# Optimization experiments

Hardware: AMD Instinct MI355X
Metric: run time of the kernel (lower is better)

The kernel has to match this reference:

```python
import jax, jax.numpy as jnp
import numpy as np

MATCH_THRESH = 0.5
NEG_POS = 3
VAR0, VAR1 = 0.1, 0.2
THETA = 0.99
NEG_INF = -1e30


def point_form(c):
    # (cx, cy, w, h) -> (x1, y1, x2, y2)
    return jnp.concatenate([c[..., :2] - c[..., 2:] / 2, c[..., :2] + c[..., 2:] / 2], -1)


def iou(a, b):
    # a: [M,4] point form, b: [A,4] point form -> [M,A]
    lt = jnp.maximum(a[:, None, :2], b[None, :, :2])
    rb = jnp.minimum(a[:, None, 2:], b[None, :, 2:])
    wh = jnp.clip(rb - lt, 0.0)
    inter = wh[..., 0] * wh[..., 1]
    area_a = ((a[:, 2] - a[:, 0]) * (a[:, 3] - a[:, 1]))[:, None]
    area_b = ((b[:, 2] - b[:, 0]) * (b[:, 3] - b[:, 1]))[None, :]
    return inter / (area_a + area_b - inter)


def encode(matched, anc):
    # matched: [A,4] point-form matched GT boxes; anc: [A,4] center form
    g_cxcy = ((matched[:, :2] + matched[:, 2:]) * 0.5 - anc[:, :2]) / (VAR0 * anc[:, 2:])
    g_wh = jnp.log((matched[:, 2:] - matched[:, :2]) / anc[:, 2:]) / VAR1
    return jnp.concatenate([g_cxcy, g_wh], -1)


def match(gt_boxes, gt_labels, anc):
    # GuaranteedEncode: SSD bipartite+threshold matching with each GT guaranteed its best anchor
    M = gt_boxes.shape[0]
    ov = iou(gt_boxes, point_form(anc))  # [M, A]
    best_gt_ov = ov.max(0)               # [A]
    best_gt_idx = ov.argmax(0)           # [A]
    best_anchor = ov.argmax(1)           # [M]
    best_gt_ov = best_gt_ov.at[best_anchor].set(2.0)
    best_gt_idx = best_gt_idx.at[best_anchor].set(jnp.arange(M))
    conf = jnp.where(best_gt_ov < MATCH_THRESH, 0, gt_labels[best_gt_idx])
    loc = encode(gt_boxes[best_gt_idx], anc)
    return conf, loc


def decode(loc, anc):
    # apply ARM deltas to anchors; keep center form for re-matching
    cxcy = anc[:, :2] + loc[:, :2] * VAR0 * anc[:, 2:]
    wh = anc[:, 2:] * jnp.exp(loc[:, 2:] * VAR1)
    return jnp.concatenate([cxcy, wh], -1)


def smooth_l1(x):
    a = jnp.abs(x)
    return jnp.where(a < 1.0, 0.5 * a * a, a - 0.5)


def ce_from_logits(logits, labels):
    return -jnp.take_along_axis(jax.nn.log_softmax(logits, -1), labels[..., None], -1)[..., 0]


def setup_inputs():
    key = jax.random.key(0)
    B, A, C, M = 32, 16320, 21, 20
    ks = jax.random.split(key, 8)
    objectness = jax.random.normal(ks[0], (B, A, 2), jnp.float32)
    refine_loc = jax.random.normal(ks[1], (B, A, 4), jnp.float32)
    pred_conf = jax.random.normal(ks[2], (B, A, C), jnp.float32)
    pred_loc = jax.random.normal(ks[3], (B, A, 4), jnp.float32)
    a_cxcy = jax.random.uniform(ks[4], (1, A, 2), jnp.float32, 0.0, 1.0)
    a_wh = jax.random.uniform(ks[5], (1, A, 2), jnp.float32, 0.05, 0.5)
    anchors = jnp.concatenate([a_cxcy, a_wh], -1)  # center form
    g_cxcy = jax.random.uniform(ks[6], (B, M, 2), jnp.float32, 0.15, 0.85)
    g_wh = jax.random.uniform(ks[7], (B, M, 2), jnp.float32, 0.05, 0.3)
    gt_boxes = jnp.concatenate([g_cxcy - g_wh / 2, g_cxcy + g_wh / 2], -1)  # point form
    gt_labels = jax.random.randint(jax.random.fold_in(key, 9), (B, M), 1, C)
    return {"objectness": objectness, "refine_loc": refine_loc, "pred_conf": pred_conf,
            "pred_loc": pred_loc, "anchors": anchors, "gt_boxes": gt_boxes, "gt_labels": gt_labels}


def reference(objectness, refine_loc, pred_conf, pred_loc, anchors, gt_boxes, gt_labels):
    B, A, C = pred_conf.shape
    anc = anchors[0]
    # --- ARM stage: match GTs to fixed anchors ---
    tconf, tloc = jax.vmap(lambda gb, gl: match(gb, gl, anc))(gt_boxes, gt_labels)  # [B,A], [B,A,4]
    pos = tconf > 0
    arm_N = jnp.sum(pos).astype(jnp.float32)
    arm_loc_loss = jnp.sum(smooth_l1(refine_loc - tloc).sum(-1) * pos)
    arm_cls_loss = jnp.sum(ce_from_logits(objectness, pos.astype(jnp.int32)))
    # --- ODM stage: re-match against ARM-refined anchors, filtered by objectness ---
    object_mask = jax.nn.softmax(objectness, -1)[..., 0] < THETA  # [B,A]
    refined = jax.vmap(lambda l: decode(l, anc))(refine_loc)       # [B,A,4] center form
    tconf2, tloc2 = jax.vmap(match)(gt_boxes, gt_labels, refined)
    tloc2 = jax.lax.stop_gradient(tloc2)  # .detach() in the original
    pos2 = (tconf2 > 0) & object_mask
    N = jnp.sum(pos2).astype(jnp.float32)
    loc_loss = jnp.sum(smooth_l1(pred_loc - tloc2).sum(-1) * pos2)
    ce = ce_from_logits(pred_conf, tconf2)  # [B,A]
    pos_num = pos2.sum(-1)                  # [B]
    neg_num = jnp.maximum(10, jnp.minimum(pos_num * NEG_POS, A - pos_num))
    neg_losses = jnp.where(object_mask & (tconf2 == 0), ce, NEG_INF)
    sorted_neg = -jnp.sort(-neg_losses, axis=-1)  # descending: hard-negative mining
    take = (jnp.arange(A)[None, :] < neg_num[:, None]) & (sorted_neg > NEG_INF / 2)
    class_loss = jnp.sum(ce * pos2) + jnp.sum(jnp.where(take, sorted_neg, 0.0))
    class_loss = class_loss / N
    loc_loss = loc_loss / N
    arm_cls_loss = 0.04 * arm_cls_loss / arm_N
    arm_loc_loss = arm_loc_loss / arm_N
    total = class_loss + loc_loss + arm_cls_loss + arm_loc_loss
    return (total, class_loss, loc_loss, arm_cls_loss, arm_loc_loss)
```

## Files before the change

### kernel.cpp

```cpp
#include <hip/hip_runtime.h>
#include <math.h>

#define MATCH_THRESH 0.5f
#define THETA 0.99f
#define NEG_INF_F (-1e30f)


__device__ __forceinline__ float iou_pf(
    float ax1, float ay1, float ax2, float ay2,
    float bx1, float by1, float bx2, float by2) {
  float lx = fmaxf(ax1, bx1), ly = fmaxf(ay1, by1);
  float rx = fminf(ax2, bx2), ry = fminf(ay2, by2);
  float w = fmaxf(rx - lx, 0.f), h = fmaxf(ry - ly, 0.f);
  float inter = w * h;
  float aa = (ax2 - ax1) * (ay2 - ay1);
  float ab = (bx2 - bx1) * (by2 - by1);
  return inter / (aa + ab - inter);
}

__device__ __forceinline__ float iou_fast(
    float ax1, float ay1, float ax2, float ay2, float aa,
    float bx1, float by1, float bx2, float by2, float ab) {
  float lx = fmaxf(ax1, bx1), ly = fmaxf(ay1, by1);
  float rx = fminf(ax2, bx2), ry = fminf(ay2, by2);
  float w = fmaxf(rx - lx, 0.f), h = fmaxf(ry - ly, 0.f);
  float inter = w * h;
  return __fdividef(inter, aa + ab - inter);
}

__device__ __forceinline__ float sl1(float x) {
  float a = fabsf(x);
  return (a < 1.f) ? 0.5f * a * a : a - 0.5f;
}

__device__ __forceinline__ float wredf(float v) {
#pragma unroll
  for (int o = 32; o > 0; o >>= 1) v += __shfl_down(v, o, 64);
  return v;
}

__device__ __forceinline__ float wredmaxf(float v) {
#pragma unroll
  for (int o = 32; o > 0; o >>= 1) v = fmaxf(v, __shfl_xor(v, o, 64));
  return v;
}

__device__ __forceinline__ int wredi(int v) {
#pragma unroll
  for (int o = 32; o > 0; o >>= 1) v += __shfl_down(v, o, 64);
  return v;
}

__device__ __forceinline__ unsigned wredmaxu(unsigned v) {
#pragma unroll
  for (int o = 32; o > 0; o >>= 1) {
    unsigned ov = __shfl_down(v, o, 64);
    v = (ov > v) ? ov : v;
  }
  return v;
}

__device__ __forceinline__ unsigned long long wredmax64(unsigned long long v) {
#pragma unroll
  for (int o = 32; o > 0; o >>= 1) {
    unsigned lo = (unsigned)v, hi = (unsigned)(v >> 32);
    unsigned olo = __shfl_down(lo, o, 64);
    unsigned ohi = __shfl_down(hi, o, 64);
    unsigned long long ov = ((unsigned long long)ohi << 32) | olo;
    v = (ov > v) ? ov : v;
  }
  return v;
}

__device__ __forceinline__ unsigned fkey(float v) {
  unsigned b = __float_as_uint(v);
  return (b & 0x80000000u) ? ~b : (b | 0x80000000u);
}
__device__ __forceinline__ float keyf(unsigned u) {
  unsigned b = (u & 0x80000000u) ? (u & 0x7fffffffu) : ~u;
  return __uint_as_float(b);
}


template <int MH>
__global__ __launch_bounds__(256) void match7_kernel(
    const float* __restrict__ gt_boxes,
    const float4* __restrict__ an4,
    const float4* __restrict__ rl4all,
    unsigned long long* __restrict__ ba1p,
    unsigned long long* __restrict__ ba2p,
    int B, int A) {
  int b = blockIdx.y;
  int half = blockIdx.z;
  const float4* rl4 = rl4all + (size_t)b * A;
  int tid = threadIdx.x;

  __shared__ float sgb[MH * 4];
  __shared__ float sarea[MH];
  if (tid < MH * 4)
    sgb[tid] = gt_boxes[((size_t)b * 2 * MH + half * MH) * 4 + tid];
  __syncthreads();
  if (tid < MH)
    sarea[tid] = (sgb[tid * 4 + 2] - sgb[tid * 4]) * (sgb[tid * 4 + 3] - sgb[tid * 4 + 1]);
  __syncthreads();

  int chunk = (A + gridDim.x - 1) / gridDim.x;
  int start = blockIdx.x * chunk;
  int end = min(start + chunk, A);

  float bvA[MH], bvR[MH];
  unsigned baA[MH], baR[MH];
#pragma unroll
  for (int m = 0; m < MH; m++) {
    bvA[m] = -1.f; baA[m] = 0u;
    bvR[m] = -1.f; baR[m] = 0u;
  }

  for (int a = start + tid; a < end; a += blockDim.x) {
    float4 an = an4[a];
    float4 rl = rl4[a];
    float ax1 = an.x - an.z * 0.5f, ay1 = an.y - an.w * 0.5f;
    float ax2 = an.x + an.z * 0.5f, ay2 = an.y + an.w * 0.5f;
    float aArea = (ax2 - ax1) * (ay2 - ay1);
    float rcx = an.x + rl.x * 0.1f * an.z;
    float rcy = an.y + rl.y * 0.1f * an.w;
    float rw = an.z * expf(rl.z * 0.2f);
    float rh = an.w * expf(rl.w * 0.2f);
    float rx1 = rcx - rw * 0.5f, ry1 = rcy - rh * 0.5f;
    float rx2 = rcx + rw * 0.5f, ry2 = rcy + rh * 0.5f;
    float rArea = (rx2 - rx1) * (ry2 - ry1);

#pragma unroll
    for (int m = 0; m < MH; m++) {
      float g0 = sgb[m * 4], g1 = sgb[m * 4 + 1], g2 = sgb[m * 4 + 2], g3 = sgb[m * 4 + 3];
      float ga = sarea[m];
      float vA = iou_fast(g0, g1, g2, g3, ga, ax1, ay1, ax2, ay2, aArea);
      if (vA > bvA[m]) { bvA[m] = vA; baA[m] = (unsigned)a; }
      float vR = iou_fast(g0, g1, g2, g3, ga, rx1, ry1, rx2, ry2, rArea);
      if (vR > bvR[m]) { bvR[m] = vR; baR[m] = (unsigned)a; }
    }
  }

  bool lane0 = (tid & 63) == 0;
#pragma unroll
  for (int m = 0; m < MH; m++) {
    {
      float vmax = wredmaxf(bvA[m]);
      unsigned cand = (bvA[m] == vmax) ? ~baA[m] : 0u;
      cand = wredmaxu(cand);
      if (lane0)
        atomicMax(&ba1p[(size_t)b * 2 * MH + half * MH + m],
                  ((unsigned long long)fkey(vmax) << 32) | cand);
    }
    {
      float vmax = wredmaxf(bvR[m]);
      unsigned cand = (bvR[m] == vmax) ? ~baR[m] : 0u;
      cand = wredmaxu(cand);
      if (lane0)
        atomicMax(&ba2p[(size_t)b * 2 * MH + half * MH + m],
                  ((unsigned long long)fkey(vmax) << 32) | cand);
    }
  }
}


__global__ __launch_bounds__(256) void gt_best_kernel(
    const float* __restrict__ gt_boxes, const float4* __restrict__ an4,
    const float4* __restrict__ rl4all, unsigned long long* __restrict__ ba1p,
    unsigned long long* __restrict__ ba2p, int B, int M, int A) {
  int bm = blockIdx.y;
  int b = bm / M;
  bool refined = (blockIdx.z == 1);
  unsigned long long* dst = refined ? ba2p : ba1p;
  const float4* rl4 = rl4all + (size_t)b * A;
  const float* g = gt_boxes + (size_t)bm * 4;
  float gx1 = g[0], gy1 = g[1], gx2 = g[2], gy2 = g[3];

  int chunk = (A + gridDim.x - 1) / gridDim.x;
  int start = blockIdx.x * chunk;
  int end = min(start + chunk, A);

  unsigned long long best = 0ull;
  for (int a = start + threadIdx.x; a < end; a += blockDim.x) {
    float4 an = an4[a];
    float cx = an.x, cy = an.y, w = an.z, h = an.w;
    if (refined) {
      float4 rl = rl4[a];
      cx += rl.x * 0.1f * w;
      cy += rl.y * 0.1f * h;
      w *= expf(rl.z * 0.2f);
      h *= expf(rl.w * 0.2f);
    }
    float v = iou_pf(gx1, gy1, gx2, gy2,
                     cx - w * 0.5f, cy - h * 0.5f, cx + w * 0.5f, cy + h * 0.5f);
    unsigned long long key =
        ((unsigned long long)fkey(v) << 32) | (unsigned)(~(unsigned)a);
    if (key > best) best = key;
  }
  best = wredmax64(best);
  __shared__ unsigned long long sm[4];
  int w = threadIdx.x >> 6;
  if ((threadIdx.x & 63) == 0) sm[w] = best;
  __syncthreads();
  if (threadIdx.x == 0) {
    unsigned long long m = sm[0];
    for (int i = 1; i < 4; i++) m = (sm[i] > m) ? sm[i] : m;
    atomicMax(&dst[bm], m);
  }
}


template <int CC>
__global__ __launch_bounds__(256) void loss_kernel(
    const float* __restrict__ gt_boxes, const int* __restrict__ gt_labels,
    const float* __restrict__ anchors, const float* __restrict__ refine_loc,
    const float* __restrict__ objectness, const float* __restrict__ pred_conf,
    const float* __restrict__ pred_loc,
    const unsigned long long* __restrict__ ba1p,
    const unsigned long long* __restrict__ ba2p,
    double* __restrict__ accB,
    int* __restrict__ armNB,
    int* __restrict__ poscnt,
    float* __restrict__ negl,
    int B, int M, int A, int C) {
  __shared__ float sgb[128];
  __shared__ float sarea[32];
  __shared__ int sb1[32], sb2[32], sgl[32];
  __shared__ float sf[4][4];
  __shared__ int sw[2][4];

  int b = blockIdx.y;
  int tid = threadIdx.x;
  if (tid < M) {
    sb1[tid] = (int)(~(unsigned)ba1p[(size_t)b * M + tid]);
    sb2[tid] = (int)(~(unsigned)ba2p[(size_t)b * M + tid]);
    sgl[tid] = gt_labels[(size_t)b * M + tid];
  }
  if (tid < M * 4) sgb[tid] = gt_boxes[(size_t)b * M * 4 + tid];
  __syncthreads();
  if (tid < M)
    sarea[tid] = (sgb[tid * 4 + 2] - sgb[tid * 4]) * (sgb[tid * 4 + 3] - sgb[tid * 4 + 1]);
  __syncthreads();

  float p_arm_loc = 0.f, p_arm_cls = 0.f, p_loc = 0.f, p_cepos = 0.f;
  int p_armN = 0, p_pos2 = 0;

  int stride = gridDim.x * blockDim.x;
#pragma unroll 2
  for (int a = blockIdx.x * blockDim.x + tid; a < A; a += stride) {
    float pr[CC > 0 ? CC : 1];
    const float* pc = pred_conf + ((size_t)b * A + a) * C;
    if constexpr (CC > 0) {
#pragma unroll
      for (int c = 0; c < CC; c++) pr[c] = pc[c];
    }
    size_t idx = (size_t)b * A + a;
    float4 an = ((const float4*)anchors)[a];
    float4 rl = ((const float4*)refine_loc)[idx];
    float2 ob = ((const float2*)objectness)[idx];

    float rcx = an.x + rl.x * 0.1f * an.z;
    float rcy = an.y + rl.y * 0.1f * an.w;
    float rw = an.z * expf(rl.z * 0.2f);
    float rh = an.w * expf(rl.w * 0.2f);

    float ax1 = an.x - an.z * 0.5f, ay1 = an.y - an.w * 0.5f;
    float ax2 = an.x + an.z * 0.5f, ay2 = an.y + an.w * 0.5f;
    float aArea = (ax2 - ax1) * (ay2 - ay1);
    float rx1 = rcx - rw * 0.5f, ry1 = rcy - rh * 0.5f;
    float rx2 = rcx + rw * 0.5f, ry2 = rcy + rh * 0.5f;
    float rArea = (rx2 - rx1) * (ry2 - ry1);
    float bestA = -1.f, bestR = -1.f;
    int biA = 0, biR = 0;
    for (int m = 0; m < M; m++) {
      float g0 = sgb[m * 4], g1 = sgb[m * 4 + 1], g2 = sgb[m * 4 + 2], g3 = sgb[m * 4 + 3];
      float ga = sarea[m];
      float vA = iou_fast(g0, g1, g2, g3, ga, ax1, ay1, ax2, ay2, aArea);
      if (vA > bestA) { bestA = vA; biA = m; }
      float vR = iou_fast(g0, g1, g2, g3, ga, rx1, ry1, rx2, ry2, rArea);
      if (vR > bestR) { bestR = vR; biR = m; }
    }
    for (int m = 0; m < M; m++) {
      if (sb1[m] == a) { biA = m; bestA = 2.f; }
      if (sb2[m] == a) { biR = m; bestR = 2.f; }
    }
    int conf1 = (bestA < MATCH_THRESH) ? 0 : sgl[biA];
    int conf2 = (bestR < MATCH_THRESH) ? 0 : sgl[biR];
    int pos1 = conf1 > 0;

    if (pos1) {
      const float* g = sgb + biA * 4;
      float gcx = ((g[0] + g[2]) * 0.5f - an.x) / (0.1f * an.z);
      float gcy = ((g[1] + g[3]) * 0.5f - an.y) / (0.1f * an.w);
      float gw = logf((g[2] - g[0]) / an.z) / 0.2f;
      float gh = logf((g[3] - g[1]) / an.w) / 0.2f;
      p_arm_loc += sl1(rl.x - gcx) + sl1(rl.y - gcy) + sl1(rl.z - gw) + sl1(rl.w - gh);
    }
    float mx = fmaxf(ob.x, ob.y);
    float e0 = __expf(ob.x - mx), e1 = __expf(ob.y - mx);
    float lse = mx + __logf(e0 + e1);
    p_arm_cls += lse - (pos1 ? ob.y : ob.x);
    p_armN += pos1;

    bool mask = (e0 / (e0 + e1)) < THETA;
    int pos2 = (conf2 > 0) && mask;

    float ce;
    if constexpr (CC > 0) {
      float mxc = pr[0];
#pragma unroll
      for (int c = 1; c < CC; c++) mxc = fmaxf(mxc, pr[c]);
      float s = 0.f;
#pragma unroll
      for (int c = 0; c < CC; c++) s += __expf(pr[c] - mxc);
      float sel = pr[0];
#pragma unroll
      for (int c = 1; c < CC; c++) sel = (conf2 == c) ? pr[c] : sel;
      ce = mxc + __logf(s) - sel;
    } else {
      float mxc = pc[0];
      float s = 1.f;
      for (int c = 1; c < C; c++) {
        float v = pc[c];
        float nm = fmaxf(mxc, v);
        s = s * __expf(mxc - nm) + __expf(v - nm);
        mxc = nm;
      }
      ce = mxc + __logf(s) - pc[conf2];
    }

    if (pos2) {
      const float* g = sgb + biR * 4;
      float gcx = ((g[0] + g[2]) * 0.5f - rcx) / (0.1f * rw);
      float gcy = ((g[1] + g[3]) * 0.5f - rcy) / (0.1f * rh);
      float gw = logf((g[2] - g[0]) / rw) / 0.2f;
      float gh = logf((g[3] - g[1]) / rh) / 0.2f;
      float4 pl = ((const float4*)pred_loc)[idx];
      p_loc += sl1(pl.x - gcx) + sl1(pl.y - gcy) + sl1(pl.z - gw) + sl1(pl.w - gh);
      p_cepos += ce;
      p_pos2 += 1;
    }
    negl[idx] = (mask && conf2 == 0) ? fmaxf(ce, 0.f) : NEG_INF_F;
  }

  p_arm_loc = wredf(p_arm_loc); p_arm_cls = wredf(p_arm_cls);
  p_loc = wredf(p_loc); p_cepos = wredf(p_cepos);
  p_armN = wredi(p_armN); p_pos2 = wredi(p_pos2);
  int w = tid >> 6;
  if ((tid & 63) == 0) {
    sf[0][w] = p_arm_loc; sf[1][w] = p_arm_cls; sf[2][w] = p_loc; sf[3][w] = p_cepos;
    sw[0][w] = p_armN; sw[1][w] = p_pos2;
  }
  __syncthreads();
  if (tid == 0) {
    float aL = 0, aC = 0, oL = 0, oC = 0;
    int aN = 0, p2 = 0;
    for (int i = 0; i < 4; i++) {
      aL += sf[0][i]; aC += sf[1][i]; oL += sf[2][i]; oC += sf[3][i];
      aN += sw[0][i]; p2 += sw[1][i];
    }
    double* ab = accB + (size_t)b * 8;
    if (aL != 0.f) atomicAdd(&ab[0], (double)aL);
    atomicAdd(&ab[1], (double)aC);
    if (oL != 0.f) atomicAdd(&ab[2], (double)oL);
    if (oC != 0.f) atomicAdd(&ab[3], (double)oC);
    if (aN) atomicAdd(&armNB[b], aN);
    if (p2) atomicAdd(&poscnt[b], p2);
  }
}


__global__ __launch_bounds__(1024) void hardneg_kernel(
    const float* __restrict__ negl, const int* __restrict__ poscnt,
    const double* __restrict__ accB, const int* __restrict__ armNB,
    double* __restrict__ acc4, int* __restrict__ ctr,
    int B, int A, float* __restrict__ out) {
  int b = blockIdx.x;
  const float* nl = negl + (size_t)b * A;
  int t = threadIdx.x;
  unsigned key[16];
#pragma unroll
  for (int j = 0; j < 16; j++) {
    int i = j * 1024 + t;
    key[j] = (i < A) ? fkey(nl[i]) : 0u;
  }
  __shared__ int wcnt[2][16];
  __shared__ float wsum[16];
  __shared__ unsigned wmax[16];
  int w = t >> 6;
  bool lane0 = (t & 63) == 0;

  const unsigned UVALID = fkey(-5e29f);
  int cv = 0;
  unsigned mk = 0;
#pragma unroll
  for (int j = 0; j < 16; j++) {
    cv += (key[j] > UVALID) ? 1 : 0;
    mk = (key[j] > mk) ? key[j] : mk;
  }
  cv = wredi(cv);
  mk = wredmaxu(mk);
  if (lane0) { wcnt[0][w] = cv; wmax[w] = mk; }
  __syncthreads();
  int cnt_valid = 0;
  unsigned maxkey = 0;
  for (int i = 0; i < 16; i++) {
    cnt_valid += wcnt[0][i];
    maxkey = (wmax[i] > maxkey) ? wmax[i] : maxkey;
  }

  int pn = poscnt[b];
  int nn = max(10, min(pn * 3, A - pn));
  int K = min(nn, cnt_valid);

  if (K > 0) {
    unsigned lo = 0x7fffffffu;
    unsigned hi = (maxkey > lo) ? maxkey : lo;
    int par = 1;
    while (lo < hi) {
      unsigned d = hi - lo;
      unsigned mid = lo + (d >> 1) + (d & 1u);
      int c = 0;
#pragma unroll
      for (int j = 0; j < 16; j++) c += (key[j] >= mid) ? 1 : 0;
      c = wredi(c);
      if (lane0) wcnt[par][w] = c;
      __syncthreads();
      int tot = 0;
      for (int i = 0; i < 16; i++) tot += wcnt[par][i];
      par ^= 1;
      if (tot >= K) {
        lo = mid;
        if (tot == K) break;
      } else hi = mid - 1;
    }

    float kth = keyf(lo);
    float sum = 0.f;
    int c1 = 0;
#pragma unroll
    for (int j = 0; j < 16; j++)
      if (key[j] > lo) { sum += keyf(key[j]); c1++; }
    sum = wredf(sum);
    c1 = wredi(c1);
    __syncthreads();
    if (lane0) { wsum[w] = sum; wcnt[0][w] = c1; }
    __syncthreads();
    if (t == 0) {
      float S = 0.f;
      int C1 = 0;
      for (int i = 0; i < 16; i++) { S += wsum[i]; C1 += wcnt[0][i]; }
      S += (float)(K - C1) * kth;
      atomicAdd(acc4, (double)S);
    }
  }

  if (t == 0) {
    __threadfence();
    int old = atomicAdd(ctr, 1);
    if (old == B - 1) {
      __threadfence();
      double arm_loc = 0, arm_cls = 0, odm_loc = 0, ce_pos = 0;
      long long Ni = 0, aNi = 0;
      for (int bb = 0; bb < B; bb++) {
        const double* ab = accB + (size_t)bb * 8;
        arm_loc += ab[0]; arm_cls += ab[1]; odm_loc += ab[2]; ce_pos += ab[3];
        Ni += poscnt[bb]; aNi += armNB[bb];
      }
      double neg_sum = *acc4;
      double N = (double)Ni, armN = (double)aNi;
      double class_loss = (ce_pos + neg_sum) / N;
      double loc_loss = odm_loc / N;
      double acls = 0.04 * arm_cls / armN;
      double aloc = arm_loc / armN;
      out[0] = (float)(class_loss + loc_loss + acls + aloc);
      out[1] = (float)class_loss;
      out[2] = (float)loc_loss;
      out[3] = (float)acls;
      out[4] = (float)aloc;
    }
  }
}


extern "C" void kernel_launch(void* const* d_in, const int* in_sizes, int n_in,
                              void* d_out, int out_size, void* d_ws, size_t ws_size,
                              hipStream_t stream) {
  const float* objectness = (const float*)d_in[0];
  const float* refine_loc = (const float*)d_in[1];
  const float* pred_conf  = (const float*)d_in[2];
  const float* pred_loc   = (const float*)d_in[3];
  const float* anchors    = (const float*)d_in[4];
  const float* gt_boxes   = (const float*)d_in[5];
  const int*   gt_labels  = (const int*)d_in[6];

  int A = in_sizes[4] / 4;
  int B = in_sizes[0] / (A * 2);
  int C = (int)(in_sizes[2] / ((long long)B * A));
  int M = in_sizes[5] / (B * 4);

  char* ws = (char*)d_ws;
  double* acc4 = (double*)ws;
  int* poscnt = (int*)(ws + 64);
  int* armNB = (int*)(ws + 192);
  int* ctr = (int*)(ws + 320);
  double* accB = (double*)(ws + 512);
  size_t ba_off = 512 + (size_t)B * 64;
  unsigned long long* ba1p = (unsigned long long*)(ws + ba_off);
  unsigned long long* ba2p = (unsigned long long*)(ws + ba_off + (size_t)B * M * 8);
  size_t zero_end = ba_off + 2 * (size_t)B * M * 8;
  size_t negl_off = (zero_end + 255) & ~(size_t)255;
  float* negl = (float*)(ws + negl_off);

  bool fast = (C == 21) && (M == 20) && (B <= 32);

  hipMemsetAsync(d_ws, 0, zero_end, stream);

  if (fast) {
    dim3 mg(16, B, 2);
    match7_kernel<10><<<mg, 256, 0, stream>>>(gt_boxes, (const float4*)anchors,
                                              (const float4*)refine_loc,
                                              ba1p, ba2p, B, A);
  } else {
    dim3 gbg(4, B * M, 2);
    gt_best_kernel<<<gbg, 256, 0, stream>>>(gt_boxes, (const float4*)anchors,
                                            (const float4*)refine_loc, ba1p, ba2p, B, M, A);
  }

  dim3 grid(32, B);
  if (C == 21) {
    loss_kernel<21><<<grid, 256, 0, stream>>>(
        gt_boxes, gt_labels, anchors, refine_loc, objectness, pred_conf, pred_loc,
        ba1p, ba2p, accB, armNB, poscnt, negl, B, M, A, C);
  } else {
    loss_kernel<0><<<grid, 256, 0, stream>>>(
        gt_boxes, gt_labels, anchors, refine_loc, objectness, pred_conf, pred_loc,
        ba1p, ba2p, accB, armNB, poscnt, negl, B, M, A, C);
  }

  hardneg_kernel<<<B, 1024, 0, stream>>>(negl, poscnt, accB, armNB, acc4, ctr,
                                         B, A, (float*)d_out);
}
```

Baseline: 111.8 us.

## Fuse matching into loss pass and correct forced best-anchor matches in fixup kernel

Folds the per-GT best-anchor search into the main loss kernel, so anchors and refine_loc are read and IoUs computed once instead of in two passes. The loss is first computed from plain threshold matching. A small fixup kernel then adjusts the accumulators and negl for each GT's forced best anchor, applying deltas for loc, class, counts and negative masking. This removes one full kernel and its memory traffic. In exchange the fused kernel holds 80 per-GT tracking registers plus 21 logits, which raises register pressure and may lower occupancy, and the delta-correction logic is more fragile.

```diff
diff --git a/kernel.cpp b/kernel.cpp
--- a/kernel.cpp
+++ b/kernel.cpp
@@ -82,46 +82,253 @@
 }
 
 
-template <int MH>
-__global__ __launch_bounds__(256) void match7_kernel(
-    const float* __restrict__ gt_boxes,
-    const float4* __restrict__ an4,
-    const float4* __restrict__ rl4all,
+template <int CC, int MM>
+__global__ __launch_bounds__(256) void lossmatch_kernel(
+    const float* __restrict__ gt_boxes, const int* __restrict__ gt_labels,
+    const float* __restrict__ anchors, const float* __restrict__ refine_loc,
+    const float* __restrict__ objectness, const float* __restrict__ pred_conf,
+    const float* __restrict__ pred_loc,
     unsigned long long* __restrict__ ba1p,
     unsigned long long* __restrict__ ba2p,
+    double* __restrict__ accB,
+    int* __restrict__ armNB,
+    int* __restrict__ poscnt,
+    float* __restrict__ negl,
     int B, int A) {
+  __shared__ float sgb[MM * 4];
+  __shared__ float sarea[MM];
+  __shared__ int sgl[MM];
+  __shared__ float sf[4][4];
+  __shared__ int sw[2][4];
+
   int b = blockIdx.y;
-  int half = blockIdx.z;
-  const float4* rl4 = rl4all + (size_t)b * A;
   int tid = threadIdx.x;
-
-  __shared__ float sgb[MH * 4];
-  __shared__ float sarea[MH];
-  if (tid < MH * 4)
-    sgb[tid] = gt_boxes[((size_t)b * 2 * MH + half * MH) * 4 + tid];
-  __syncthreads();
-  if (tid < MH)
+  if (tid < MM) sgl[tid] = gt_labels[(size_t)b * MM + tid];
+  if (tid < MM * 4) sgb[tid] = gt_boxes[(size_t)b * MM * 4 + tid];
+  __syncthreads();
+  if (tid < MM)
     sarea[tid] = (sgb[tid * 4 + 2] - sgb[tid * 4]) * (sgb[tid * 4 + 3] - sgb[tid * 4 + 1]);
   __syncthreads();
 
-  int chunk = (A + gridDim.x - 1) / gridDim.x;
-  int start = blockIdx.x * chunk;
-  int end = min(start + chunk, A);
-
-  float bvA[MH], bvR[MH];
-  unsigned baA[MH], baR[MH];
-#pragma unroll
-  for (int m = 0; m < MH; m++) {
+  float p_arm_loc = 0.f, p_arm_cls = 0.f, p_loc = 0.f, p_cepos = 0.f;
+  int p_armN = 0, p_pos2 = 0;
+
+  float bvA[MM], bvR[MM];
+  unsigned baA[MM], baR[MM];
+#pragma unroll
+  for (int m = 0; m < MM; m++) {
     bvA[m] = -1.f; baA[m] = 0u;
     bvR[m] = -1.f; baR[m] = 0u;
   }
 
-  for (int a = start + tid; a < end; a += blockDim.x) {
-    float4 an = an4[a];
-    float4 rl = rl4[a];
+  int stride = gridDim.x * blockDim.x;
+  for (int a = blockIdx.x * blockDim.x + tid; a < A; a += stride) {
+    float pr[CC];
+    const float* pc = pred_conf + ((size_t)b * A + a) * CC;
+#pragma unroll
+    for (int c = 0; c < CC; c++) pr[c] = pc[c];
+
+    size_t idx = (size_t)b * A + a;
+    float4 an = ((const float4*)anchors)[a];
+    float4 rl = ((const float4*)refine_loc)[idx];
+    float2 ob = ((const float2*)objectness)[idx];
+
+    float rcx = an.x + rl.x * 0.1f * an.z;
+    float rcy = an.y + rl.y * 0.1f * an.w;
+    float rw = an.z * expf(rl.z * 0.2f);
+    float rh = an.w * expf(rl.w * 0.2f);
+
     float ax1 = an.x - an.z * 0.5f, ay1 = an.y - an.w * 0.5f;
     float ax2 = an.x + an.z * 0.5f, ay2 = an.y + an.w * 0.5f;
     float aArea = (ax2 - ax1) * (ay2 - ay1);
+    float rx1 = rcx - rw * 0.5f, ry1 = rcy - rh * 0.5f;
+    float rx2 = rcx + rw * 0.5f, ry2 = rcy + rh * 0.5f;
+    float rArea = (rx2 - rx1) * (ry2 - ry1);
+
+    float bestA = -1.f, bestR = -1.f;
+    int biA = 0, biR = 0;
+#pragma unroll
+    for (int m = 0; m < MM; m++) {
+      float g0 = sgb[m * 4], g1 = sgb[m * 4 + 1], g2 = sgb[m * 4 + 2], g3 = sgb[m * 4 + 3];
+      float ga = sarea[m];
+      float vA = iou_fast(g0, g1, g2, g3, ga, ax1, ay1, ax2, ay2, aArea);
+      if (vA > bestA) { bestA = vA; biA = m; }
+      if (vA > bvA[m]) { bvA[m] = vA; baA[m] = (unsigned)a; }
+      float vR = iou_fast(g0, g1, g2, g3, ga, rx1, ry1, rx2, ry2, rArea);
+      if (vR > bestR) { bestR = vR; biR = m; }
+      if (vR > bvR[m]) { bvR[m] = vR; baR[m] = (unsigned)a; }
+    }
+    int conf1 = (bestA < MATCH_THRESH) ? 0 : sgl[biA];
+    int conf2 = (bestR < MATCH_THRESH) ? 0 : sgl[biR];
+    int pos1 = conf1 > 0;
+
+    if (pos1) {
+      const float* g = sgb + biA * 4;
+      float gcx = ((g[0] + g[2]) * 0.5f - an.x) / (0.1f * an.z);
+      float gcy = ((g[1] + g[3]) * 0.5f - an.y) / (0.1f * an.w);
+      float gw = logf((g[2] - g[0]) / an.z) / 0.2f;
+      float gh = logf((g[3] - g[1]) / an.w) / 0.2f;
+      p_arm_loc += sl1(rl.x - gcx) + sl1(rl.y - gcy) + sl1(rl.z - gw) + sl1(rl.w - gh);
+    }
+    float mx = fmaxf(ob.x, ob.y);
+    float e0 = __expf(ob.x - mx), e1 = __expf(ob.y - mx);
+    float lse = mx + __logf(e0 + e1);
+    p_arm_cls += lse - (pos1 ? ob.y : ob.x);
+    p_armN += pos1;
+
+    bool mask = (e0 / (e0 + e1)) < THETA;
+    int pos2 = (conf2 > 0) && mask;
+
+    float mxc = pr[0];
+#pragma unroll
+    for (int c = 1; c < CC; c++) mxc = fmaxf(mxc, pr[c]);
+    float s = 0.f;
+#pragma unroll
+    for (int c = 0; c < CC; c++) s += __expf(pr[c] - mxc);
+    float sel = pr[0];
+#pragma unroll
+    for (int c = 1; c < CC; c++) sel = (conf2 == c) ? pr[c] : sel;
+    float ce = mxc + __logf(s) - sel;
+
+    if (pos2) {
+      const float* g = sgb + biR * 4;
+      float gcx = ((g[0] + g[2]) * 0.5f - rcx) / (0.1f * rw);
+      float gcy = ((g[1] + g[3]) * 0.5f - rcy) / (0.1f * rh);
+      float gw = logf((g[2] - g[0]) / rw) / 0.2f;
+      float gh = logf((g[3] - g[1]) / rh) / 0.2f;
+      float4 pl = ((const float4*)pred_loc)[idx];
+      p_loc += sl1(pl.x - gcx) + sl1(pl.y - gcy) + sl1(pl.z - gw) + sl1(pl.w - gh);
+      p_cepos += ce;
+      p_pos2 += 1;
+    }
+    negl[idx] = (mask && conf2 == 0) ? fmaxf(ce, 0.f) : NEG_INF_F;
+  }
+
+  p_arm_loc = wredf(p_arm_loc); p_arm_cls = wredf(p_arm_cls);
+  p_loc = wredf(p_loc); p_cepos = wredf(p_cepos);
+  p_armN = wredi(p_armN); p_pos2 = wredi(p_pos2);
+  int w = tid >> 6;
+  if ((tid & 63) == 0) {
+    sf[0][w] = p_arm_loc; sf[1][w] = p_arm_cls; sf[2][w] = p_loc; sf[3][w] = p_cepos;
+    sw[0][w] = p_armN; sw[1][w] = p_pos2;
+  }
+  __syncthreads();
+  if (tid == 0) {
+    float aL = 0, aC = 0, oL = 0, oC = 0;
+    int aN = 0, p2 = 0;
+    for (int i = 0; i < 4; i++) {
+      aL += sf[0][i]; aC += sf[1][i]; oL += sf[2][i]; oC += sf[3][i];
+      aN += sw[0][i]; p2 += sw[1][i];
+    }
+    double* ab = accB + (size_t)b * 8;
+    if (aL != 0.f) atomicAdd(&ab[0], (double)aL);
+    atomicAdd(&ab[1], (double)aC);
+    if (oL != 0.f) atomicAdd(&ab[2], (double)oL);
+    if (oC != 0.f) atomicAdd(&ab[3], (double)oC);
+    if (aN) atomicAdd(&armNB[b], aN);
+    if (p2) atomicAdd(&poscnt[b], p2);
+  }
+
+  bool lane0 = (tid & 63) == 0;
+#pragma unroll
+  for (int m = 0; m < MM; m++) {
+    {
+      float vmax = wredmaxf(bvA[m]);
+      unsigned cand = (bvA[m] == vmax) ? ~baA[m] : 0u;
+      cand = wredmaxu(cand);
+      if (lane0)
+        atomicMax(&ba1p[(size_t)b * MM + m],
+                  ((unsigned long long)fkey(vmax) << 32) | cand);
+    }
+    {
+      float vmax = wredmaxf(bvR[m]);
+      unsigned cand = (bvR[m] == vmax) ? ~baR[m] : 0u;
+      cand = wredmaxu(cand);
+      if (lane0)
+        atomicMax(&ba2p[(size_t)b * MM + m],
+                  ((unsigned long long)fkey(vmax) << 32) | cand);
+    }
+  }
+}
+
+
+template <int CC, int MM>
+__global__ void fixup_kernel(
+    const float* __restrict__ gt_boxes, const int* __restrict__ gt_labels,
+    const float* __restrict__ anchors, const float* __restrict__ refine_loc,
+    const float* __restrict__ objectness, const float* __restrict__ pred_conf,
+    const float* __restrict__ pred_loc,
+    const unsigned long long* __restrict__ ba1p,
+    const unsigned long long* __restrict__ ba2p,
+    double* __restrict__ accB, int* __restrict__ armNB, int* __restrict__ poscnt,
+    float* __restrict__ negl, int B, int A) {
+  int b = blockIdx.x;
+  int stage = blockIdx.y;
+  int tid = threadIdx.x;
+  __shared__ float sgb[MM * 4];
+  __shared__ float sarea[MM];
+  __shared__ int sgl[MM];
+  __shared__ int sa[MM];
+  const unsigned long long* bap = (stage ? ba2p : ba1p) + (size_t)b * MM;
+  if (tid < MM * 4) sgb[tid] = gt_boxes[(size_t)b * MM * 4 + tid];
+  if (tid < MM) {
+    sgl[tid] = gt_labels[(size_t)b * MM + tid];
+    sa[tid] = (int)(~(unsigned)bap[tid]);
+  }
+  __syncthreads();
+  if (tid < MM)
+    sarea[tid] = (sgb[tid * 4 + 2] - sgb[tid * 4]) * (sgb[tid * 4 + 3] - sgb[tid * 4 + 1]);
+  __syncthreads();
+  if (tid >= MM) return;
+  int a = sa[tid];
+  for (int m2 = tid + 1; m2 < MM; m2++)
+    if (sa[m2] == a) return;
+
+  size_t idx = (size_t)b * A + a;
+  float4 an = ((const float4*)anchors)[a];
+  float4 rl = ((const float4*)refine_loc)[idx];
+  float2 ob = ((const float2*)objectness)[idx];
+  float mx = fmaxf(ob.x, ob.y);
+  float e0 = __expf(ob.x - mx), e1 = __expf(ob.y - mx);
+
+  if (stage == 0) {
+    float ax1 = an.x - an.z * 0.5f, ay1 = an.y - an.w * 0.5f;
+    float ax2 = an.x + an.z * 0.5f, ay2 = an.y + an.w * 0.5f;
+    float aArea = (ax2 - ax1) * (ay2 - ay1);
+    float bestA = -1.f;
+    int biA = 0;
+#pragma unroll
+    for (int m = 0; m < MM; m++) {
+      float vA = iou_fast(sgb[m * 4], sgb[m * 4 + 1], sgb[m * 4 + 2], sgb[m * 4 + 3],
+                          sarea[m], ax1, ay1, ax2, ay2, aArea);
+      if (vA > bestA) { bestA = vA; biA = m; }
+    }
+    int conf1b = (bestA < MATCH_THRESH) ? 0 : sgl[biA];
+    int p1b = conf1b > 0;
+    float locB = 0.f;
+    if (p1b) {
+      const float* g = sgb + biA * 4;
+      float gcx = ((g[0] + g[2]) * 0.5f - an.x) / (0.1f * an.z);
+      float gcy = ((g[1] + g[3]) * 0.5f - an.y) / (0.1f * an.w);
+      float gw = logf((g[2] - g[0]) / an.z) / 0.2f;
+      float gh = logf((g[3] - g[1]) / an.w) / 0.2f;
+      locB = sl1(rl.x - gcx) + sl1(rl.y - gcy) + sl1(rl.z - gw) + sl1(rl.w - gh);
+    }
+    float locA;
+    {
+      const float* g = sgb + tid * 4;
+      float gcx = ((g[0] + g[2]) * 0.5f - an.x) / (0.1f * an.z);
+      float gcy = ((g[1] + g[3]) * 0.5f - an.y) / (0.1f * an.w);
+      float gw = logf((g[2] - g[0]) / an.z) / 0.2f;
+      float gh = logf((g[3] - g[1]) / an.w) / 0.2f;
+      locA = sl1(rl.x - gcx) + sl1(rl.y - gcy) + sl1(rl.z - gw) + sl1(rl.w - gh);
+    }
+    float clsDelta = (p1b ? ob.y : ob.x) - ob.y;
+    double* ab = accB + (size_t)b * 8;
+    atomicAdd(&ab[0], (double)(locA - locB));
+    if (clsDelta != 0.f) atomicAdd(&ab[1], (double)clsDelta);
+    if (!p1b) atomicAdd(&armNB[b], 1);
+  } else {
     float rcx = an.x + rl.x * 0.1f * an.z;
     float rcy = an.y + rl.y * 0.1f * an.w;
     float rw = an.z * expf(rl.z * 0.2f);
@@ -129,37 +336,66 @@
     float rx1 = rcx - rw * 0.5f, ry1 = rcy - rh * 0.5f;
     float rx2 = rcx + rw * 0.5f, ry2 = rcy + rh * 0.5f;
     float rArea = (rx2 - rx1) * (ry2 - ry1);
-
-#pragma unroll
-    for (int m = 0; m < MH; m++) {
-      float g0 = sgb[m * 4], g1 = sgb[m * 4 + 1], g2 = sgb[m * 4 + 2], g3 = sgb[m * 4 + 3];
-      float ga = sarea[m];
-      float vA = iou_fast(g0, g1, g2, g3, ga, ax1, ay1, ax2, ay2, aArea);
-      if (vA > bvA[m]) { bvA[m] = vA; baA[m] = (unsigned)a; }
-      float vR = iou_fast(g0, g1, g2, g3, ga, rx1, ry1, rx2, ry2, rArea);
-      if (vR > bvR[m]) { bvR[m] = vR; baR[m] = (unsigned)a; }
-    }
-  }
-
-  bool lane0 = (tid & 63) == 0;
-#pragma unroll
-  for (int m = 0; m < MH; m++) {
-    {
-      float vmax = wredmaxf(bvA[m]);
-      unsigned cand = (bvA[m] == vmax) ? ~baA[m] : 0u;
-      cand = wredmaxu(cand);
-      if (lane0)
-        atomicMax(&ba1p[(size_t)b * 2 * MH + half * MH + m],
-                  ((unsigned long long)fkey(vmax) << 32) | cand);
-    }
-    {
-      float vmax = wredmaxf(bvR[m]);
-      unsigned cand = (bvR[m] == vmax) ? ~baR[m] : 0u;
-      cand = wredmaxu(cand);
-      if (lane0)
-        atomicMax(&ba2p[(size_t)b * 2 * MH + half * MH + m],
-                  ((unsigned long long)fkey(vmax) << 32) | cand);
-    }
+    float bestR = -1.f;
+    int biR = 0;
+#pragma unroll
+    for (int m = 0; m < MM; m++) {
+      float vR = iou_fast(sgb[m * 4], sgb[m * 4 + 1], sgb[m * 4 + 2], sgb[m * 4 + 3],
+                          sarea[m], rx1, ry1, rx2, ry2, rArea);
+      if (vR > bestR) { bestR = vR; biR = m; }
+    }
+    int conf2b = (bestR < MATCH_THRESH) ? 0 : sgl[biR];
+    bool mask = (e0 / (e0 + e1)) < THETA;
+    int p2b = (conf2b > 0) && mask;
+    int p2a = mask ? 1 : 0;
+
+    float pr[CC];
+    const float* pc = pred_conf + idx * CC;
+#pragma unroll
+    for (int c = 0; c < CC; c++) pr[c] = pc[c];
+    float mxc = pr[0];
+#pragma unroll
+    for (int c = 1; c < CC; c++) mxc = fmaxf(mxc, pr[c]);
+    float s = 0.f;
+#pragma unroll
+    for (int c = 0; c < CC; c++) s += __expf(pr[c] - mxc);
+    float lse21 = mxc + __logf(s);
+    float selB = pr[0], selA = pr[0];
+    int conf2a = sgl[tid];
+#pragma unroll
+    for (int c = 1; c < CC; c++) {
+      selB = (conf2b == c) ? pr[c] : selB;
+      selA = (conf2a == c) ? pr[c] : selA;
+    }
+    float ceb = lse21 - selB;
+    float cea = lse21 - selA;
+
+    float locB = 0.f, locA = 0.f;
+    float4 pl = ((const float4*)pred_loc)[idx];
+    if (p2b) {
+      const float* g = sgb + biR * 4;
+      float gcx = ((g[0] + g[2]) * 0.5f - rcx) / (0.1f * rw);
+      float gcy = ((g[1] + g[3]) * 0.5f - rcy) / (0.1f * rh);
+      float gw = logf((g[2] - g[0]) / rw) / 0.2f;
+      float gh = logf((g[3] - g[1]) / rh) / 0.2f;
+      locB = sl1(pl.x - gcx) + sl1(pl.y - gcy) + sl1(pl.z - gw) + sl1(pl.w - gh);
+    }
+    if (p2a) {
+      const float* g = sgb + tid * 4;
+      float gcx = ((g[0] + g[2]) * 0.5f - rcx) / (0.1f * rw);
+      float gcy = ((g[1] + g[3]) * 0.5f - rcy) / (0.1f * rh);
+      float gw = logf((g[2] - g[0]) / rw) / 0.2f;
+      float gh = logf((g[3] - g[1]) / rh) / 0.2f;
+      locA = sl1(pl.x - gcx) + sl1(pl.y - gcy) + sl1(pl.z - gw) + sl1(pl.w - gh);
+    }
+    float dLoc = locA - locB;
+    float dCe = (p2a ? cea : 0.f) - (p2b ? ceb : 0.f);
+    int dP = p2a - p2b;
+    double* ab = accB + (size_t)b * 8;
+    if (dLoc != 0.f) atomicAdd(&ab[2], (double)dLoc);
+    if (dCe != 0.f) atomicAdd(&ab[3], (double)dCe);
+    if (dP) atomicAdd(&poscnt[b], dP);
+    negl[idx] = NEG_INF_F;
   }
 }
 
@@ -209,22 +445,16 @@
   }
 }
 
-
-template <int CC>
-__global__ __launch_bounds__(256) void loss_kernel(
+__global__ __launch_bounds__(256) void loss_fb_kernel(
     const float* __restrict__ gt_boxes, const int* __restrict__ gt_labels,
     const float* __restrict__ anchors, const float* __restrict__ refine_loc,
     const float* __restrict__ objectness, const float* __restrict__ pred_conf,
     const float* __restrict__ pred_loc,
     const unsigned long long* __restrict__ ba1p,
     const unsigned long long* __restrict__ ba2p,
-    double* __restrict__ accB,
-    int* __restrict__ armNB,
-    int* __restrict__ poscnt,
-    float* __restrict__ negl,
-    int B, int M, int A, int C) {
+    double* __restrict__ accB, int* __restrict__ armNB, int* __restrict__ poscnt,
+    float* __restrict__ negl, int B, int M, int A, int C) {
   __shared__ float sgb[128];
-  __shared__ float sarea[32];
   __shared__ int sb1[32], sb2[32], sgl[32];
   __shared__ float sf[4][4];
   __shared__ int sw[2][4];
@@ -238,23 +468,14 @@
   }
   if (tid < M * 4) sgb[tid] = gt_boxes[(size_t)b * M * 4 + tid];
   __syncthreads();
-  if (tid < M)
-    sarea[tid] = (sgb[tid * 4 + 2] - sgb[tid * 4]) * (sgb[tid * 4 + 3] - sgb[tid * 4 + 1]);
-  __syncthreads();
 
   float p_arm_loc = 0.f, p_arm_cls = 0.f, p_loc = 0.f, p_cepos = 0.f;
   int p_armN = 0, p_pos2 = 0;
 
   int stride = gridDim.x * blockDim.x;
-#pragma unroll 2
   for (int a = blockIdx.x * blockDim.x + tid; a < A; a += stride) {
-    float pr[CC > 0 ? CC : 1];
-    const float* pc = pred_conf + ((size_t)b * A + a) * C;
-    if constexpr (CC > 0) {
-#pragma unroll
-      for (int c = 0; c < CC; c++) pr[c] = pc[c];
-    }
     size_t idx = (size_t)b * A + a;
+    const float* pc = pred_conf + idx * C;
     float4 an = ((const float4*)anchors)[a];
     float4 rl = ((const float4*)refine_loc)[idx];
     float2 ob = ((const float2*)objectness)[idx];
@@ -266,18 +487,15 @@
 
     float ax1 = an.x - an.z * 0.5f, ay1 = an.y - an.w * 0.5f;
     float ax2 = an.x + an.z * 0.5f, ay2 = an.y + an.w * 0.5f;
-    float aArea = (ax2 - ax1) * (ay2 - ay1);
     float rx1 = rcx - rw * 0.5f, ry1 = rcy - rh * 0.5f;
     float rx2 = rcx + rw * 0.5f, ry2 = rcy + rh * 0.5f;
-    float rArea = (rx2 - rx1) * (ry2 - ry1);
     float bestA = -1.f, bestR = -1.f;
     int biA = 0, biR = 0;
     for (int m = 0; m < M; m++) {
       float g0 = sgb[m * 4], g1 = sgb[m * 4 + 1], g2 = sgb[m * 4 + 2], g3 = sgb[m * 4 + 3];
-      float ga = sarea[m];
-      float vA = iou_fast(g0, g1, g2, g3, ga, ax1, ay1, ax2, ay2, aArea);
+      float vA = iou_pf(g0, g1, g2, g3, ax1, ay1, ax2, ay2);
       if (vA > bestA) { bestA = vA; biA = m; }
-      float vR = iou_fast(g0, g1, g2, g3, ga, rx1, ry1, rx2, ry2, rArea);
+      float vR = iou_pf(g0, g1, g2, g3, rx1, ry1, rx2, ry2);
       if (vR > bestR) { bestR = vR; biR = m; }
     }
     for (int m = 0; m < M; m++) {
@@ -305,29 +523,15 @@
     bool mask = (e0 / (e0 + e1)) < THETA;
     int pos2 = (conf2 > 0) && mask;
 
-    float ce;
-    if constexpr (CC > 0) {
-      float mxc = pr[0];
-#pragma unroll
-      for (int c = 1; c < CC; c++) mxc = fmaxf(mxc, pr[c]);
-      float s = 0.f;
-#pragma unroll
-      for (int c = 0; c < CC; c++) s += __expf(pr[c] - mxc);
-      float sel = pr[0];
-#pragma unroll
-      for (int c = 1; c < CC; c++) sel = (conf2 == c) ? pr[c] : sel;
-      ce = mxc + __logf(s) - sel;
-    } else {
-      float mxc = pc[0];
-      float s = 1.f;
-      for (int c = 1; c < C; c++) {
-        float v = pc[c];
-        float nm = fmaxf(mxc, v);
-        s = s * __expf(mxc - nm) + __expf(v - nm);
-        mxc = nm;
-      }
-      ce = mxc + __logf(s) - pc[conf2];
-    }
+    float mxc = pc[0];
+    float s = 1.f;
+    for (int c = 1; c < C; c++) {
+      float v = pc[c];
+      float nm = fmaxf(mxc, v);
+      s = s * __expf(mxc - nm) + __expf(v - nm);
+      mxc = nm;
+    }
+    float ce = mxc + __logf(s) - pc[conf2];
 
     if (pos2) {
       const float* g = sgb + biR * 4;
@@ -517,25 +721,22 @@
   hipMemsetAsync(d_ws, 0, zero_end, stream);
 
   if (fast) {
-    dim3 mg(16, B, 2);
-    match7_kernel<10><<<mg, 256, 0, stream>>>(gt_boxes, (const float4*)anchors,
-                                              (const float4*)refine_loc,
-                                              ba1p, ba2p, B, A);
+    dim3 grid(32, B);
+    lossmatch_kernel<21, 20><<<grid, 256, 0, stream>>>(
+        gt_boxes, gt_labels, anchors, refine_loc, objectness, pred_conf, pred_loc,
+        ba1p, ba2p, accB, armNB, poscnt, negl, B, A);
+    dim3 fg(B, 2);
+    fixup_kernel<21, 20><<<fg, 64, 0, stream>>>(
+        gt_boxes, gt_labels, anchors, refine_loc, objectness, pred_conf, pred_loc,
+        ba1p, ba2p, accB, armNB, poscnt, negl, B, A);
   } else {
     dim3 gbg(4, B * M, 2);
     gt_best_kernel<<<gbg, 256, 0, stream>>>(gt_boxes, (const float4*)anchors,
                                             (const float4*)refine_loc, ba1p, ba2p, B, M, A);
-  }
-
-  dim3 grid(32, B);
-  if (C == 21) {
-    loss_kernel<21><<<grid, 256, 0, stream>>>(
+    dim3 grid(32, B);
+    loss_fb_kernel<<<grid, 256, 0, stream>>>(
         gt_boxes, gt_labels, anchors, refine_loc, objectness, pred_conf, pred_loc,
         ba1p, ba2p, accB, armNB, poscnt, negl, B, M, A, C);
-  } else {
-    loss_kernel<0><<<grid, 256, 0, stream>>>(
-        gt_boxes, gt_labels, anchors, refine_loc, objectness, pred_conf, pred_loc,
-        ba1p, ba2p, accB, armNB, poscnt, negl, B, M, A, C);
   }
 
   hardneg_kernel<<<B, 1024, 0, stream>>>(negl, poscnt, accB, armNB, acc4, ctr,
```

Result: slower. 179.9 us (+60.9%).
